# Performance work log

Measured on AMD Instinct MI355X. Metric: run time of the kernel, lower is better.

The kernel has to match this reference:

```python
import jax, jax.numpy as jnp
import numpy as np

B, S, D = 16, 512, 384
MAX_DUR = 16  # durations drawn from [0, 16)


def setup_inputs() -> dict:
    key = jax.random.key(0)
    k1, k2 = jax.random.split(key)
    hidden = jax.random.normal(k1, (B, S, D), dtype=jnp.float32)
    durations = jax.random.randint(k2, (B, S), 0, MAX_DUR, dtype=jnp.int32)
    return {"hidden": hidden, "durations": durations}


def reference(hidden, durations):
    # hidden: [B, S, D], durations: [B, S] int
    out_lengths = durations.sum(axis=1)              # [B]
    # NOTE: output length is data-dependent (matches torch eager semantics);
    # concretize it here. Under jit one would pass a static max_length instead.
    max_length = int(out_lengths.max())
    csum = jnp.cumsum(durations, axis=1)             # [B, S] inclusive cumsum
    pos = jnp.arange(max_length)                     # [L]
    # Output frame j of batch b copies token t where csum[b,t-1] <= j < csum[b,t]
    # (tokens with duration 0 are skipped automatically by side='right').
    idx = jax.vmap(lambda c: jnp.searchsorted(c, pos, side='right'))(csum)  # [B, L]
    idx = jnp.minimum(idx, hidden.shape[1] - 1)      # clamp padding region
    out = jnp.take_along_axis(hidden, idx[:, :, None], axis=1)  # [B, L, D]
    # zero out positions beyond each batch's expanded length (torch init zeros)
    valid = (pos[None, :] < out_lengths[:, None]).astype(hidden.dtype)  # [B, L]
    out = out * valid[:, :, None]
    return out, out_lengths
```

## Files before the change

### kernel.cpp

```cpp
#include <hip/hip_runtime.h>

#define NB 16
#define NS 512
#define ND 384
#define K4 (ND/4)
#define ROWS 16
#define NT 256

__global__ __launch_bounds__(NT) void length_regulator_fused(
    const float4* __restrict__ hidden4,
    const int*    __restrict__ dur,
    float4*       __restrict__ out4,
    float*        __restrict__ outLenF,
    int L)
{
    const int t = threadIdx.x;
    const int b = blockIdx.y;
    const int chunk = blockIdx.x;
    const int j0 = chunk * ROWS;

    __shared__ int csum[NS];
    __shared__ int wsum[NT / 64];
    __shared__ int rowTok[ROWS];

    int2 d2 = ((const int2*)(dur + b * NS))[t];
    int local = d2.x + d2.y;
    int lane = t & 63, wave = t >> 6;
    int x = local;
    #pragma unroll
    for (int off = 1; off < 64; off <<= 1) {
        int y = __shfl_up(x, off, 64);
        if (lane >= off) x += y;
    }
    if (lane == 63) wsum[wave] = x;
    __syncthreads();
    if (t == 0) {
        int acc = 0;
        #pragma unroll
        for (int w = 0; w < NT / 64; ++w) { int tmp = wsum[w]; wsum[w] = acc; acc += tmp; }
    }
    __syncthreads();
    int excl = wsum[wave] + x - local;
    csum[2 * t]     = excl + d2.x;
    csum[2 * t + 1] = excl + local;
    __syncthreads();

    const int total = csum[NS - 1];

    if (chunk == 0 && t == 0) outLenF[b] = (float)total;

    if (t < ROWS) {
        int j = j0 + t;
        int g = -1;
        if (j < L && j < total) {
            int lo = 0, hi = NS;
            while (lo < hi) {
                int mid = (lo + hi) >> 1;
                if (csum[mid] <= j) lo = mid + 1; else hi = mid;
            }
            if (lo > NS - 1) lo = NS - 1;
            g = lo;
        }
        rowTok[t] = g;
    }
    __syncthreads();

    const size_t outBase = ((size_t)b * L + j0) * K4;
    #pragma unroll
    for (int i = t; i < ROWS * K4; i += NT) {
        int r = i / K4;
        int k = i - r * K4;
        int j = j0 + r;
        if (j >= L) break;
        int g = rowTok[r];
        float4 v;
        if (g < 0) v = make_float4(0.f, 0.f, 0.f, 0.f);
        else       v = hidden4[(size_t)(b * NS + g) * K4 + k];
        out4[outBase + i] = v;
    }
}

extern "C" void kernel_launch(void* const* d_in, const int* in_sizes, int n_in,
                              void* d_out, int out_size, void* d_ws, size_t ws_size,
                              hipStream_t stream) {
    const float* hidden   = (const float*)d_in[0];
    const int*   durations = (const int*)d_in[1];
    float* out = (float*)d_out;

    int L = (out_size - NB) / (NB * ND);
    float* outLenF = out + (size_t)NB * L * ND;

    dim3 grid((L + ROWS - 1) / ROWS, NB);
    length_regulator_fused<<<grid, NT, 0, stream>>>(
        (const float4*)hidden, durations, (float4*)out, outLenF, L);
}
```

Baseline: 118.8 us.

## Scatter token indices directly from scan and enlarge rows per block

Each block now covers 64 output rows instead of 16, so the duration scan is repeated across four times fewer blocks. The shared cumsum array and per-row binary search are replaced by each thread writing its own tokens' frame ranges into a row-to-token table. A serial wave-offset step and its barrier are dropped, since every thread sums the wave totals itself. In exchange there are fewer blocks overall, and the scatter loop can run long for threads whose tokens have large durations.

Measured after the change: 122.1 us. 1.03x slower.

```diff
diff --git a/kernel.cpp b/kernel.cpp
--- a/kernel.cpp
+++ b/kernel.cpp
@@ -4,7 +4,7 @@
 #define NS 512
 #define ND 384
 #define K4 (ND/4)
-#define ROWS 16
+#define ROWS 64
 #define NT 256
 
 __global__ __launch_bounds__(NT) void length_regulator_fused(
@@ -16,12 +16,12 @@
 {
     const int t = threadIdx.x;
     const int b = blockIdx.y;
-    const int chunk = blockIdx.x;
-    const int j0 = chunk * ROWS;
+    const int j0 = blockIdx.x * ROWS;
 
-    __shared__ int csum[NS];
     __shared__ int wsum[NT / 64];
     __shared__ int rowTok[ROWS];
+
+    if (t < ROWS) rowTok[t] = -1;
 
     int2 d2 = ((const int2*)(dur + b * NS))[t];
     int local = d2.x + d2.y;
@@ -34,48 +34,37 @@
     }
     if (lane == 63) wsum[wave] = x;
     __syncthreads();
-    if (t == 0) {
-        int acc = 0;
-        #pragma unroll
-        for (int w = 0; w < NT / 64; ++w) { int tmp = wsum[w]; wsum[w] = acc; acc += tmp; }
+    int wbase = 0, total = 0;
+    #pragma unroll
+    for (int w = 0; w < NT / 64; ++w) {
+        int s = wsum[w];
+        if (w < wave) wbase += s;
+        total += s;
     }
-    __syncthreads();
-    int excl = wsum[wave] + x - local;
-    csum[2 * t]     = excl + d2.x;
-    csum[2 * t + 1] = excl + local;
-    __syncthreads();
+    int excl = wbase + x - local;
 
-    const int total = csum[NS - 1];
-
-    if (chunk == 0 && t == 0) outLenF[b] = (float)total;
-
-    if (t < ROWS) {
-        int j = j0 + t;
-        int g = -1;
-        if (j < L && j < total) {
-            int lo = 0, hi = NS;
-            while (lo < hi) {
-                int mid = (lo + hi) >> 1;
-                if (csum[mid] <= j) lo = mid + 1; else hi = mid;
-            }
-            if (lo > NS - 1) lo = NS - 1;
-            g = lo;
-        }
-        rowTok[t] = g;
+    {
+        int e0 = excl,        n0 = d2.x;
+        int e1 = excl + d2.x, n1 = d2.y;
+        int lo0 = max(e0, j0), hi0 = min(e0 + n0, j0 + ROWS);
+        for (int j = lo0; j < hi0; ++j) rowTok[j - j0] = 2 * t;
+        int lo1 = max(e1, j0), hi1 = min(e1 + n1, j0 + ROWS);
+        for (int j = lo1; j < hi1; ++j) rowTok[j - j0] = 2 * t + 1;
     }
     __syncthreads();
 
+    if (j0 == 0 && t == 0) outLenF[b] = (float)total;
+
     const size_t outBase = ((size_t)b * L + j0) * K4;
-    #pragma unroll
+    const size_t hidBase = (size_t)b * NS * K4;
     for (int i = t; i < ROWS * K4; i += NT) {
         int r = i / K4;
         int k = i - r * K4;
-        int j = j0 + r;
-        if (j >= L) break;
+        if (j0 + r >= L) break;
         int g = rowTok[r];
         float4 v;
         if (g < 0) v = make_float4(0.f, 0.f, 0.f, 0.f);
-        else       v = hidden4[(size_t)(b * NS + g) * K4 + k];
+        else       v = hidden4[hidBase + (size_t)g * K4 + k];
         out4[outBase + i] = v;
     }
 }
@@ -83,7 +72,7 @@
 extern "C" void kernel_launch(void* const* d_in, const int* in_sizes, int n_in,
                               void* d_out, int out_size, void* d_ws, size_t ws_size,
                               hipStream_t stream) {
-    const float* hidden   = (const float*)d_in[0];
+    const float* hidden    = (const float*)d_in[0];
     const int*   durations = (const int*)d_in[1];
     float* out = (float*)d_out;
 
```
